# Optimization experiments

Hardware: AMD Instinct MI355X
Metric: run time of the kernel (lower is better)

## Reference

```python
import jax, jax.numpy as jnp
import numpy as np

B, S, H = 2, 2048, 4096
NQ, NKV, D = 32, 8, 128
EPS = 1e-6
THETA = 1000000.0


def rms_norm(x, w, eps=EPS):
    # normalize over last dim (per-head RMSNorm on head_dim)
    var = jnp.mean(jnp.square(x), axis=-1, keepdims=True)
    return x * jax.lax.rsqrt(var + eps) * w


def rope(x, positions, theta=THETA):
    # x: [B, S, N, D]; rotate-half convention (Qwen/Llama style)
    d = x.shape[-1]
    inv_freq = 1.0 / (theta ** (jnp.arange(0, d, 2, dtype=jnp.float32) / d))  # [D/2]
    ang = positions[:, None].astype(jnp.float32) * inv_freq[None, :]          # [S, D/2]
    cos = jnp.cos(ang)[None, :, None, :]
    sin = jnp.sin(ang)[None, :, None, :]
    x1, x2 = x[..., : d // 2], x[..., d // 2 :]
    return jnp.concatenate([x1 * cos - x2 * sin, x2 * cos + x1 * sin], axis=-1)


def setup_inputs() -> dict:
    key = jax.random.key(0)
    ks = jax.random.split(key, 7)
    sc_in = 1.0 / np.sqrt(H)
    sc_out = 1.0 / np.sqrt(NQ * D)
    return {
        "x": jax.random.normal(ks[0], (B, S, H), jnp.float32),
        "wq": jax.random.normal(ks[1], (H, NQ * D), jnp.float32) * sc_in,
        "wk": jax.random.normal(ks[2], (H, NKV * D), jnp.float32) * sc_in,
        "wv": jax.random.normal(ks[3], (H, NKV * D), jnp.float32) * sc_in,
        "wo": jax.random.normal(ks[4], (NQ * D, H), jnp.float32) * sc_out,
        "q_norm_w": jnp.ones((D,), jnp.float32),
        "k_norm_w": jnp.ones((D,), jnp.float32),
    }


def reference(x, wq, wk, wv, wo, q_norm_w, k_norm_w):
    b, s, _ = x.shape
    positions = jnp.arange(s)

    q = (x @ wq).reshape(b, s, NQ, D)   # [B,S,NQ,D]
    k = (x @ wk).reshape(b, s, NKV, D)  # [B,S,NKV,D]
    v = (x @ wv).reshape(b, s, NKV, D)

    # per-head QK RMSNorm, then RoPE
    q = rope(rms_norm(q, q_norm_w), positions)
    k = rope(rms_norm(k, k_norm_w), positions)

    # GQA: expand kv heads to query heads (group = NQ // NKV)
    g = NQ // NKV
    k = jnp.repeat(k, g, axis=2)  # [B,S,NQ,D]
    v = jnp.repeat(v, g, axis=2)

    scale = D ** -0.5
    scores = jnp.einsum("bqhd,bkhd->bhqk", q, k) * scale  # [B,NQ,S,S]
    causal = jnp.tril(jnp.ones((s, s), bool))
    scores = jnp.where(causal[None, None], scores, jnp.finfo(scores.dtype).min)
    attn = jax.nn.softmax(scores, axis=-1)

    out = jnp.einsum("bhqk,bkhd->bqhd", attn, v).reshape(b, s, NQ * D)
    return out @ wo
```

## Files before the change

kernel.cpp:

```cpp
#include <hip/hip_runtime.h>
#include <hip/hip_bf16.h>

#define DEV __device__ __forceinline__

typedef unsigned short u16;
typedef unsigned int u32;
typedef __attribute__((ext_vector_type(8))) short short8;
typedef __attribute__((ext_vector_type(4))) float f32x4;
typedef __attribute__((ext_vector_type(16))) float f32x16;

static constexpr int Bb = 2, Ss = 2048, Hh = 4096, NQ = 32, NKV = 8, Dd = 128;
static constexpr int Mm = Bb * Ss;

DEV u16 f2bf(float f) {
    u32 u = __float_as_uint(f);
    u32 r = (u + 0x7fffu + ((u >> 16) & 1u)) >> 16;
    return (u16)r;
}
DEV float bf2f(u16 b) { return __uint_as_float((u32)b << 16); }
DEV u32 cvtpk(float lo, float hi) {
    u32 r;
    asm("v_cvt_pk_bf16_f32 %0, %1, %2" : "=v"(r) : "v"(lo), "v"(hi));
    return r;
}

__global__ void k_cast(const float4* __restrict__ in, ushort4* __restrict__ out, int n4) {
    int i = blockIdx.x * 256 + threadIdx.x;
    if (i < n4) {
        float4 v = in[i];
        ushort4 o;
        o.x = f2bf(v.x); o.y = f2bf(v.y); o.z = f2bf(v.z); o.w = f2bf(v.w);
        out[i] = o;
    }
}

__global__ void k_transpose(const float* __restrict__ in, u16* __restrict__ out, int R, int C) {
    __shared__ float t[32][33];
    int lx = threadIdx.x & 31, ly = threadIdx.x >> 5;
    long tc = (long)blockIdx.x * 32, tr = (long)blockIdx.y * 32;
    #pragma unroll
    for (int i = 0; i < 32; i += 8) t[ly + i][lx] = in[(tr + ly + i) * C + tc + lx];
    __syncthreads();
    #pragma unroll
    for (int i = 0; i < 32; i += 8) out[(tc + ly + i) * R + tr + lx] = f2bf(t[lx][ly + i]);
}

DEV void gld16(const void* g, void* l) {
    __builtin_amdgcn_global_load_lds((const __attribute__((address_space(1))) void*)g,
                                     (__attribute__((address_space(3))) void*)l, 16, 0, 0);
}

#define FENCE asm volatile("" ::: "memory")

template <int MODE>
__global__ __launch_bounds__(512) void k_gemm256(const u16* __restrict__ A, const u16* __restrict__ B0,
                                                 const u16* __restrict__ B1, void* __restrict__ C0,
                                                 void* __restrict__ C1, void* __restrict__ C2,
                                                 int M, int N, int K, int nbx) {
    __shared__ u16 S[2][32768];
    const int tid = threadIdx.x, lane = tid & 63, wid = tid >> 6;
    const int wr = wid >> 2, wc = wid & 3;
    const int l = blockIdx.x;
    const int bx = l % nbx, by = l / nbx;
    const long m0 = (long)by * 256, n0 = (long)bx * 256;
    const int r15 = lane & 15;
    const int cch0 = 8 * ((lane >> 4) ^ (r15 & 7));

    const u16* Bbase = B0;
    long nb0 = n0;
    if (MODE == 3 && bx >= 16) { Bbase = B1; nb0 = n0 - 4096; }

    const u16 *pA[4], *pB[4];
    {
        int srow = wid * 8 + (lane >> 3);
        int scol = 8 * ((lane & 7) ^ (lane >> 3));
        #pragma unroll
        for (int j = 0; j < 4; j++) {
            pA[j] = A + (m0 + j * 64 + srow) * (long)K + scol;
            pB[j] = Bbase + (nb0 + j * 64 + srow) * (long)K + scol;
        }
    }

    f32x4 acc[8][4];
    #pragma unroll
    for (int i = 0; i < 8; i++)
        #pragma unroll
        for (int j = 0; j < 4; j++) acc[i][j] = f32x4{0.f, 0.f, 0.f, 0.f};

    const int NT = K / 64;
    auto STAGE_A = [&](int t) {
        int tb = t & 1; long ko = (long)t * 64;
        #pragma unroll
        for (int j = 0; j < 4; j++) gld16(pA[j] + ko, (void*)&S[tb][j * 4096 + wid * 512]);
    };
    auto STAGE_B = [&](int t) {
        int tb = t & 1; long ko = (long)t * 64;
        #pragma unroll
        for (int j = 0; j < 4; j++) gld16(pB[j] + ko, (void*)&S[tb][16384 + j * 4096 + wid * 512]);
    };

    const int aro = wr * 8192 + r15 * 64 + cch0;
    const int bro = 16384 + (wc >> 1) * 8192 + (wc & 1) * 4096 + r15 * 64 + cch0;

    STAGE_B(0); STAGE_A(0); STAGE_B(1); STAGE_A(1);
    asm volatile("s_waitcnt vmcnt(8)" ::: "memory");
    FENCE; __builtin_amdgcn_s_barrier(); FENCE;

    short8 af[4][2], b01[2][2], b23[2][2];
    for (int kt = 0; kt < NT; ++kt) {
        const u16* Sb = S[kt & 1];
        #pragma unroll
        for (int m = 0; m < 4; m++) {
            af[m][0] = *(const short8*)&Sb[aro + m * 1024];
            af[m][1] = *(const short8*)&Sb[(aro + m * 1024) ^ 32];
        }
        #pragma unroll
        for (int n = 0; n < 2; n++) {
            b01[n][0] = *(const short8*)&Sb[bro + n * 1024];
            b01[n][1] = *(const short8*)&Sb[(bro + n * 1024) ^ 32];
        }
        __builtin_amdgcn_s_setprio(1);
        #pragma unroll
        for (int m = 0; m < 4; m++)
            #pragma unroll
            for (int n = 0; n < 2; n++) {
                acc[m][n] = __builtin_amdgcn_mfma_f32_16x16x32_bf16(af[m][0], b01[n][0], acc[m][n], 0, 0, 0);
                acc[m][n] = __builtin_amdgcn_mfma_f32_16x16x32_bf16(af[m][1], b01[n][1], acc[m][n], 0, 0, 0);
            }
        __builtin_amdgcn_s_setprio(0);
        #pragma unroll
        for (int n = 0; n < 2; n++) {
            b23[n][0] = *(const short8*)&Sb[bro + (n + 2) * 1024];
            b23[n][1] = *(const short8*)&Sb[(bro + (n + 2) * 1024) ^ 32];
        }
        __builtin_amdgcn_s_setprio(1);
        #pragma unroll
        for (int m = 0; m < 4; m++)
            #pragma unroll
            for (int n = 0; n < 2; n++) {
                acc[m][n + 2] = __builtin_amdgcn_mfma_f32_16x16x32_bf16(af[m][0], b23[n][0], acc[m][n + 2], 0, 0, 0);
                acc[m][n + 2] = __builtin_amdgcn_mfma_f32_16x16x32_bf16(af[m][1], b23[n][1], acc[m][n + 2], 0, 0, 0);
            }
        __builtin_amdgcn_s_setprio(0);
        FENCE; __builtin_amdgcn_s_barrier(); FENCE;
        if (kt + 2 < NT) STAGE_B(kt + 2);
        #pragma unroll
        for (int m = 0; m < 4; m++) {
            af[m][0] = *(const short8*)&Sb[aro + (m + 4) * 1024];
            af[m][1] = *(const short8*)&Sb[(aro + (m + 4) * 1024) ^ 32];
        }
        __builtin_amdgcn_s_setprio(1);
        #pragma unroll
        for (int m = 0; m < 4; m++)
            #pragma unroll
            for (int n = 0; n < 2; n++) {
                acc[m + 4][n] = __builtin_amdgcn_mfma_f32_16x16x32_bf16(af[m][0], b01[n][0], acc[m + 4][n], 0, 0, 0);
                acc[m + 4][n] = __builtin_amdgcn_mfma_f32_16x16x32_bf16(af[m][1], b01[n][1], acc[m + 4][n], 0, 0, 0);
            }
        __builtin_amdgcn_s_setprio(0);
        FENCE; __builtin_amdgcn_s_barrier(); FENCE;
        if (kt + 2 < NT) {
            STAGE_A(kt + 2);
            asm volatile("s_waitcnt vmcnt(8)" ::: "memory");
        } else {
            asm volatile("s_waitcnt vmcnt(0)" ::: "memory");
        }
        __builtin_amdgcn_s_setprio(1);
        #pragma unroll
        for (int m = 0; m < 4; m++)
            #pragma unroll
            for (int n = 0; n < 2; n++) {
                acc[m + 4][n + 2] = __builtin_amdgcn_mfma_f32_16x16x32_bf16(af[m][0], b23[n][0], acc[m + 4][n + 2], 0, 0, 0);
                acc[m + 4][n + 2] = __builtin_amdgcn_mfma_f32_16x16x32_bf16(af[m][1], b23[n][1], acc[m + 4][n + 2], 0, 0, 0);
            }
        __builtin_amdgcn_s_setprio(0);
        FENCE; __builtin_amdgcn_s_barrier(); FENCE;
    }

    const int rq = (lane >> 4) * 4;
    #pragma unroll
    for (int m = 0; m < 8; m++) {
        #pragma unroll
        for (int n = 0; n < 4; n++) {
            long row0 = m0 + wr * 128 + m * 16 + rq;
            long col = n0 + wc * 64 + n * 16 + r15;
            if (MODE == 0) {
                float* Cf = (float*)C0;
                #pragma unroll
                for (int i = 0; i < 4; i++) Cf[(row0 + i) * N + col] = acc[m][n][i];
            } else if (MODE == 2) {
                u16* Cb = (u16*)C0;
                #pragma unroll
                for (int i = 0; i < 4; i++) Cb[(row0 + i) * N + col] = f2bf(acc[m][n][i]);
            } else {
                if (bx < 16) {
                    u16* Cb = (u16*)C0;
                    #pragma unroll
                    for (int i = 0; i < 4; i++) Cb[(row0 + i) * 4096 + col] = f2bf(acc[m][n][i]);
                } else if (bx < 20) {
                    u16* Cb = (u16*)C1;
                    long cl = col - 4096;
                    #pragma unroll
                    for (int i = 0; i < 4; i++) Cb[(row0 + i) * 1024 + cl] = f2bf(acc[m][n][i]);
                } else {
                    u16* Cb = (u16*)C2;
                    long cl = col - 5120;
                    ushort4 pk;
                    pk.x = f2bf(acc[m][n][0]);
                    pk.y = f2bf(acc[m][n][1]);
                    pk.z = f2bf(acc[m][n][2]);
                    pk.w = f2bf(acc[m][n][3]);
                    *(ushort4*)&Cb[cl * Mm + row0] = pk;
                }
            }
        }
    }
}

__global__ __launch_bounds__(256) void k_normrope(u16* __restrict__ buf,
                                                  const float* __restrict__ w, int NH, float oscale) {
    int row = blockIdx.x * 4 + (threadIdx.x >> 6);
    int lane = threadIdx.x & 63;
    long base = (long)row * 128;
    float x1 = bf2f(buf[base + lane]), x2 = bf2f(buf[base + lane + 64]);
    float ss = x1 * x1 + x2 * x2;
    #pragma unroll
    for (int m = 1; m < 64; m <<= 1) ss += __shfl_xor(ss, m);
    float r = rsqrtf(ss * (1.f / 128.f) + 1e-6f);
    float n1 = x1 * r * w[lane], n2 = x2 * r * w[lane + 64];
    int pos = (row / NH) % Ss;
    float invf = exp2f((float)lane * (-19.931568569324174f / 64.f));
    float ang = (float)pos * invf;
    float c = cosf(ang), sn = sinf(ang);
    buf[base + lane] = f2bf((n1 * c - n2 * sn) * oscale);
    buf[base + lane + 64] = f2bf((n2 * c + n1 * sn) * oscale);
}

__global__ __launch_bounds__(256, 2) void k_attn(const u16* __restrict__ Q, const u16* __restrict__ Kb,
                                                 const u16* __restrict__ Vg, u16* __restrict__ O) {
    __shared__ u16 KT[2][64 * 128];
    __shared__ u16 VT[2][128 * 64];
    int tid = threadIdx.x, lane = tid & 63, wid = tid >> 6;
    int d0 = blockIdx.x;
    int L = (d0 & 7) * 64 + (d0 >> 3);
    int pr = L & 31;
    int hk = (L >> 5) & 7;
    int b = L >> 8;
    int h = hk * 4 + wid;
    int q0a = pr * 32;
    int q0b = (63 - pr) * 32;
    int c31 = lane & 31, hi5 = lane >> 5;
    int kx16 = (c31 & 15) << 3;
    int kx8 = (c31 & 7) << 3;

    short8 qfa[8], qfb[8];
    {
        const u16* qra = Q + ((long)(b * Ss + q0a + c31) * NQ + h) * Dd + hi5 * 8;
        const u16* qrb = Q + ((long)(b * Ss + q0b + c31) * NQ + h) * Dd + hi5 * 8;
        #pragma unroll
        for (int c = 0; c < 8; c++) {
            qfa[c] = *(const short8*)(qra + c * 16);
            qfb[c] = *(const short8*)(qrb + c * 16);
        }
    }

    const u16* kg[4];
    const u16* vg[4];
    int i0 = wid * 4;
    #pragma unroll
    for (int ii = 0; ii < 4; ii++) {
        int i = i0 + ii;
        int r = i * 4 + (lane >> 4);
        kg[ii] = Kb + ((long)(b * Ss + r) * NKV + hk) * Dd + 8 * ((lane & 15) ^ (r & 15));
        int d = i * 8 + (lane >> 3);
        vg[ii] = Vg + (long)(hk * Dd + d) * Mm + (long)b * Ss + 8 * ((lane & 7) ^ (d & 7));
    }

    f32x16 oaa[4], oab[4];
    #pragma unroll
    for (int f = 0; f < 4; f++)
        #pragma unroll
        for (int r = 0; r < 16; r++) { oaa[f][r] = 0.f; oab[f][r] = 0.f; }
    float mra = -INFINITY, lra = 0.f, mrb = -INFINITY, lrb = 0.f;

    const long kadv = (long)64 * NKV * Dd;
    int nt = q0b / 64 + 1;
    int cur = 0;

    auto STEP = [&](int k0, int q0, const short8 (&qf)[8], f32x16 (&oa)[4],
                    float& mrun, float& lrun) {
        int ql = q0 + c31;
        int krow = k0 & 32;
        f32x16 st;
        #pragma unroll
        for (int r = 0; r < 16; r++) st[r] = 0.f;
        __builtin_amdgcn_s_setprio(1);
        #pragma unroll
        for (int c = 0; c < 8; c++) {
            short8 kf = *(const short8*)&KT[cur][(krow + c31) * 128 + ((c * 16 + hi5 * 8) ^ kx16)];
            st = __builtin_amdgcn_mfma_f32_32x32x16_bf16(kf, qf[c], st, 0, 0, 0);
        }
        __builtin_amdgcn_s_setprio(0);
        float p[16];
        if (k0 + 31 > q0) {
            #pragma unroll
            for (int r = 0; r < 16; r++) {
                int kidx = k0 + (r & 3) + 8 * (r >> 2) + 4 * hi5;
                p[r] = (kidx > ql) ? -INFINITY : st[r];
            }
        } else {
            #pragma unroll
            for (int r = 0; r < 16; r++) p[r] = st[r];
        }
        float pmax = p[0];
        #pragma unroll
        for (int r = 1; r < 16; r++) pmax = fmaxf(pmax, p[r]);
        pmax = fmaxf(pmax, __shfl_xor(pmax, 32));
        if (!__all(pmax - mrun <= 8.f)) {
            float mnew = fmaxf(mrun, pmax);
            float sc = __builtin_amdgcn_exp2f(mrun - mnew);
            lrun *= sc;
            #pragma unroll
            for (int f = 0; f < 4; f++)
                #pragma unroll
                for (int r = 0; r < 16; r++) oa[f][r] *= sc;
            mrun = mnew;
        }
        float ls = 0.f;
        #pragma unroll
        for (int r = 0; r < 16; r++) {
            float e = __builtin_amdgcn_exp2f(p[r] - mrun);
            p[r] = e;
            ls += e;
        }
        ls += __shfl_xor(ls, 32);
        lrun += ls;

        u32 w0 = cvtpk(p[0], p[1]), w1 = cvtpk(p[2], p[3]);
        u32 w2 = cvtpk(p[4], p[5]), w3 = cvtpk(p[6], p[7]);
        u32 w4 = cvtpk(p[8], p[9]), w5 = cvtpk(p[10], p[11]);
        u32 w6 = cvtpk(p[12], p[13]), w7 = cvtpk(p[14], p[15]);
        u32 x0 = (u32)__shfl_xor((int)w0, 32), x1 = (u32)__shfl_xor((int)w1, 32);
        u32 x2 = (u32)__shfl_xor((int)w2, 32), x3 = (u32)__shfl_xor((int)w3, 32);
        u32 x4 = (u32)__shfl_xor((int)w4, 32), x5 = (u32)__shfl_xor((int)w5, 32);
        u32 x6 = (u32)__shfl_xor((int)w6, 32), x7 = (u32)__shfl_xor((int)w7, 32);
        union { u32 u[4]; short8 s; } pb0, pb1;
        if (hi5) {
            pb0.u[0] = x2; pb0.u[1] = x3; pb0.u[2] = w2; pb0.u[3] = w3;
            pb1.u[0] = x6; pb1.u[1] = x7; pb1.u[2] = w6; pb1.u[3] = w7;
        } else {
            pb0.u[0] = w0; pb0.u[1] = w1; pb0.u[2] = x0; pb0.u[3] = x1;
            pb1.u[0] = w4; pb1.u[1] = w5; pb1.u[2] = x4; pb1.u[3] = x5;
        }
        __builtin_amdgcn_s_setprio(1);
        #pragma unroll
        for (int f = 0; f < 4; f++) {
            int d = 32 * f + c31;
            const u16* vrow = &VT[cur][d * 64];
            short8 v0 = *(const short8*)&vrow[(krow + hi5 * 8) ^ kx8];
            short8 v1 = *(const short8*)&vrow[(krow + 16 + hi5 * 8) ^ kx8];
            oa[f] = __builtin_amdgcn_mfma_f32_32x32x16_bf16(v0, pb0.s, oa[f], 0, 0, 0);
            oa[f] = __builtin_amdgcn_mfma_f32_32x32x16_bf16(v1, pb1.s, oa[f], 0, 0, 0);
        }
        __builtin_amdgcn_s_setprio(0);
    };

    #pragma unroll
    for (int ii = 0; ii < 4; ii++) {
        gld16(kg[ii], &KT[0][(i0 + ii) * 512]);
        gld16(vg[ii], &VT[0][(i0 + ii) * 512]);
    }
    __syncthreads();

    for (int t = 0; t < nt; ++t) {
        if (t + 1 < nt) {
            long ko = (long)(t + 1) * kadv;
            int vo = (t + 1) * 64;
            #pragma unroll
            for (int ii = 0; ii < 4; ii++) {
                gld16(kg[ii] + ko, &KT[cur ^ 1][(i0 + ii) * 512]);
                gld16(vg[ii] + vo, &VT[cur ^ 1][(i0 + ii) * 512]);
            }
        }
        #pragma unroll
        for (int ks = 0; ks < 2; ++ks) {
            int k0 = t * 64 + ks * 32;
            if (k0 <= q0a + 31) STEP(k0, q0a, qfa, oaa, mra, lra);
            if (k0 <= q0b + 31) STEP(k0, q0b, qfb, oab, mrb, lrb);
        }
        __syncthreads();
        cur ^= 1;
    }

    #pragma unroll
    for (int x = 0; x < 2; x++) {
        int q0 = x ? q0b : q0a;
        f32x16* oa = x ? oab : oaa;
        float linv = 1.f / (x ? lrb : lra);
        u16* orow = O + ((long)(b * Ss + q0 + c31) * NQ + h) * Dd;
        #pragma unroll
        for (int f = 0; f < 4; f++) {
            #pragma unroll
            for (int rq = 0; rq < 4; rq++) {
                int dbase = 32 * f + 8 * rq + 4 * hi5;
                union { u32 u[2]; ushort4 v; } pk;
                pk.u[0] = cvtpk(oa[f][4 * rq + 0] * linv, oa[f][4 * rq + 1] * linv);
                pk.u[1] = cvtpk(oa[f][4 * rq + 2] * linv, oa[f][4 * rq + 3] * linv);
                *(ushort4*)(orow + dbase) = pk.v;
            }
        }
    }
}

extern "C" void kernel_launch(void* const* d_in, const int* in_sizes, int n_in,
                              void* d_out, int out_size, void* d_ws, size_t ws_size,
                              hipStream_t stream) {
    (void)in_sizes; (void)n_in; (void)out_size; (void)ws_size;
    const float* x = (const float*)d_in[0];
    const float* wq = (const float*)d_in[1];
    const float* wk = (const float*)d_in[2];
    const float* wv = (const float*)d_in[3];
    const float* wo = (const float*)d_in[4];
    const float* qnw = (const float*)d_in[5];
    const float* knw = (const float*)d_in[6];

    char* ws = (char*)d_ws;
    const size_t MB = 1024 * 1024;
    const float qscale = (float)(0.08838834764831845 * 1.4426950408889634);

    u16* xb = (u16*)(ws);
    u16* Wq = (u16*)(ws + 32 * MB);
    u16* qb = (u16*)(ws + 64 * MB);
    u16* kb = (u16*)(ws + 96 * MB);
    u16* vt = (u16*)(ws + 104 * MB);
    u16* ao = xb;
    u16* Wkv = (u16*)(ws + 112 * MB);
    u16* WkT = Wkv;
    u16* WvT = Wkv + (size_t)1024 * 4096;

    int n4 = Mm * Hh / 4;
    k_cast<<<n4 / 256, 256, 0, stream>>>((const float4*)x, (ushort4*)xb, n4);

    k_transpose<<<dim3(Hh / 32, Hh / 32), 256, 0, stream>>>(wq, Wq, Hh, Hh);
    k_transpose<<<dim3((NKV * Dd) / 32, Hh / 32), 256, 0, stream>>>(wk, WkT, Hh, NKV * Dd);
    k_transpose<<<dim3((NKV * Dd) / 32, Hh / 32), 256, 0, stream>>>(wv, WvT, Hh, NKV * Dd);

    k_gemm256<3><<<24 * (Mm / 256), 512, 0, stream>>>(xb, Wq, Wkv, qb, kb, vt, Mm, 6144, Hh, 24);

    k_normrope<<<(Mm * NQ) / 4, 256, 0, stream>>>(qb, qnw, NQ, qscale);
    k_normrope<<<(Mm * NKV) / 4, 256, 0, stream>>>(kb, knw, NKV, 1.0f);

    k_attn<<<512, 256, 0, stream>>>(qb, kb, vt, ao);

    k_transpose<<<dim3(Hh / 32, Hh / 32), 256, 0, stream>>>(wo, Wq, Hh, Hh);
    k_gemm256<0><<<16 * (Mm / 256), 512, 0, stream>>>(ao, Wq, nullptr, d_out, nullptr, nullptr, Mm, Hh, NQ * Dd, 16);
}
```

Measured before the change: 552.1 us.

## Use 256x192 tiles for fused QKV GEMM with contiguous concatenated weight buffer

The QKV projection GEMM now uses a 256x192 output tile (NF=3 fragments per wave column) instead of 256x256, which raises the grid from 384 to 512 blocks. That gives a whole number of waves on the CU count and better load balance. Wq, Wk and Wv are transposed into one contiguous buffer, so the second B pointer and the bx-based branch are gone and output routing is done per column. The K loop is simplified from four MFMA phases to three, and the vmcnt wait count is parameterised. The trade-off is lower arithmetic intensity per block and more total A-tile reloads.

New measurement: 540.4 us. 1.02x faster.

```diff
diff --git a/kernel.cpp b/kernel.cpp
--- a/kernel.cpp
+++ b/kernel.cpp
@@ -54,59 +54,57 @@
 
 template <int MODE>
 __global__ __launch_bounds__(512) void k_gemm256(const u16* __restrict__ A, const u16* __restrict__ B0,
-                                                 const u16* __restrict__ B1, void* __restrict__ C0,
-                                                 void* __restrict__ C1, void* __restrict__ C2,
-                                                 int M, int N, int K, int nbx) {
-    __shared__ u16 S[2][32768];
+                                                 void* __restrict__ C0, void* __restrict__ C1,
+                                                 void* __restrict__ C2, int M, int N, int K, int nbx) {
+    constexpr int NF = (MODE == 3) ? 3 : 4;
+    constexpr int LPT = 4 + NF;
+    __shared__ u16 S[2][16384 + NF * 4096];
     const int tid = threadIdx.x, lane = tid & 63, wid = tid >> 6;
     const int wr = wid >> 2, wc = wid & 3;
     const int l = blockIdx.x;
     const int bx = l % nbx, by = l / nbx;
-    const long m0 = (long)by * 256, n0 = (long)bx * 256;
+    const long m0 = (long)by * 256, n0 = (long)bx * (NF * 64);
     const int r15 = lane & 15;
     const int cch0 = 8 * ((lane >> 4) ^ (r15 & 7));
 
-    const u16* Bbase = B0;
-    long nb0 = n0;
-    if (MODE == 3 && bx >= 16) { Bbase = B1; nb0 = n0 - 4096; }
-
-    const u16 *pA[4], *pB[4];
+    const u16 *pA[4], *pB[NF];
     {
-        int srow = wid * 8 + (lane >> 3);
-        int scol = 8 * ((lane & 7) ^ (lane >> 3));
-        #pragma unroll
-        for (int j = 0; j < 4; j++) {
-            pA[j] = A + (m0 + j * 64 + srow) * (long)K + scol;
-            pB[j] = Bbase + (nb0 + j * 64 + srow) * (long)K + scol;
-        }
-    }
-
-    f32x4 acc[8][4];
+        int rl = lane >> 3;
+        int sc = 8 * ((lane & 7) ^ rl);
+        #pragma unroll
+        for (int j = 0; j < 4; j++)
+            pA[j] = A + (m0 + (wid * 4 + j) * 8 + rl) * (long)K + sc;
+        #pragma unroll
+        for (int j = 0; j < NF; j++)
+            pB[j] = B0 + (n0 + (wid * NF + j) * 8 + rl) * (long)K + sc;
+    }
+
+    f32x4 acc[8][NF];
     #pragma unroll
     for (int i = 0; i < 8; i++)
         #pragma unroll
-        for (int j = 0; j < 4; j++) acc[i][j] = f32x4{0.f, 0.f, 0.f, 0.f};
+        for (int j = 0; j < NF; j++) acc[i][j] = f32x4{0.f, 0.f, 0.f, 0.f};
 
     const int NT = K / 64;
     auto STAGE_A = [&](int t) {
         int tb = t & 1; long ko = (long)t * 64;
         #pragma unroll
-        for (int j = 0; j < 4; j++) gld16(pA[j] + ko, (void*)&S[tb][j * 4096 + wid * 512]);
+        for (int j = 0; j < 4; j++) gld16(pA[j] + ko, (void*)&S[tb][(wid * 4 + j) * 512]);
     };
     auto STAGE_B = [&](int t) {
         int tb = t & 1; long ko = (long)t * 64;
         #pragma unroll
-        for (int j = 0; j < 4; j++) gld16(pB[j] + ko, (void*)&S[tb][16384 + j * 4096 + wid * 512]);
+        for (int j = 0; j < NF; j++) gld16(pB[j] + ko, (void*)&S[tb][16384 + (wid * NF + j) * 512]);
     };
 
     const int aro = wr * 8192 + r15 * 64 + cch0;
-    const int bro = 16384 + (wc >> 1) * 8192 + (wc & 1) * 4096 + r15 * 64 + cch0;
+    const int bro = 16384 + wc * (NF * 1024) + r15 * 64 + cch0;
 
     STAGE_B(0); STAGE_A(0); STAGE_B(1); STAGE_A(1);
-    asm volatile("s_waitcnt vmcnt(8)" ::: "memory");
+    asm volatile("s_waitcnt vmcnt(%0)" ::"i"(LPT) : "memory");
     FENCE; __builtin_amdgcn_s_barrier(); FENCE;
 
-    short8 af[4][2], b01[2][2], b23[2][2];
+    short8 af[4][2], bf[NF][2];
     for (int kt = 0; kt < NT; ++kt) {
         const u16* Sb = S[kt & 1];
         #pragma unroll
@@ -115,31 +113,17 @@
             af[m][1] = *(const short8*)&Sb[(aro + m * 1024) ^ 32];
         }
         #pragma unroll
-        for (int n = 0; n < 2; n++) {
-            b01[n][0] = *(const short8*)&Sb[bro + n * 1024];
-            b01[n][1] = *(const short8*)&Sb[(bro + n * 1024) ^ 32];
+        for (int n = 0; n < NF; n++) {
+            bf[n][0] = *(const short8*)&Sb[bro + n * 1024];
+            bf[n][1] = *(const short8*)&Sb[(bro + n * 1024) ^ 32];
         }
         __builtin_amdgcn_s_setprio(1);
         #pragma unroll
         for (int m = 0; m < 4; m++)
             #pragma unroll
-            for (int n = 0; n < 2; n++) {
-                acc[m][n] = __builtin_amdgcn_mfma_f32_16x16x32_bf16(af[m][0], b01[n][0], acc[m][n], 0, 0, 0);
-                acc[m][n] = __builtin_amdgcn_mfma_f32_16x16x32_bf16(af[m][1], b01[n][1], acc[m][n], 0, 0, 0);
-            }
-        __builtin_amdgcn_s_setprio(0);
-        #pragma unroll
-        for (int n = 0; n < 2; n++) {
-            b23[n][0] = *(const short8*)&Sb[bro + (n + 2) * 1024];
-            b23[n][1] = *(const short8*)&Sb[(bro + (n + 2) * 1024) ^ 32];
-        }
-        __builtin_amdgcn_s_setprio(1);
-        #pragma unroll
-        for (int m = 0; m < 4; m++)
-            #pragma unroll
-            for (int n = 0; n < 2; n++) {
-                acc[m][n + 2] = __builtin_amdgcn_mfma_f32_16x16x32_bf16(af[m][0], b23[n][0], acc[m][n + 2], 0, 0, 0);
-                acc[m][n + 2] = __builtin_amdgcn_mfma_f32_16x16x32_bf16(af[m][1], b23[n][1], acc[m][n + 2], 0, 0, 0);
+            for (int n = 0; n < NF; n++) {
+                acc[m][n] = __builtin_amdgcn_mfma_f32_16x16x32_bf16(af[m][0], bf[n][0], acc[m][n], 0, 0, 0);
+                acc[m][n] = __builtin_amdgcn_mfma_f32_16x16x32_bf16(af[m][1], bf[n][1], acc[m][n], 0, 0, 0);
             }
         __builtin_amdgcn_s_setprio(0);
         FENCE; __builtin_amdgcn_s_barrier(); FENCE;
@@ -153,27 +137,18 @@
         #pragma unroll
         for (int m = 0; m < 4; m++)
             #pragma unroll
-            for (int n = 0; n < 2; n++) {
-                acc[m + 4][n] = __builtin_amdgcn_mfma_f32_16x16x32_bf16(af[m][0], b01[n][0], acc[m + 4][n], 0, 0, 0);
-                acc[m + 4][n] = __builtin_amdgcn_mfma_f32_16x16x32_bf16(af[m][1], b01[n][1], acc[m + 4][n], 0, 0, 0);
+            for (int n = 0; n < NF; n++) {
+                acc[m + 4][n] = __builtin_amdgcn_mfma_f32_16x16x32_bf16(af[m][0], bf[n][0], acc[m + 4][n], 0, 0, 0);
+                acc[m + 4][n] = __builtin_amdgcn_mfma_f32_16x16x32_bf16(af[m][1], bf[n][1], acc[m + 4][n], 0, 0, 0);
             }
         __builtin_amdgcn_s_setprio(0);
         FENCE; __builtin_amdgcn_s_barrier(); FENCE;
         if (kt + 2 < NT) {
             STAGE_A(kt + 2);
-            asm volatile("s_waitcnt vmcnt(8)" ::: "memory");
+            asm volatile("s_waitcnt vmcnt(%0)" ::"i"(LPT) : "memory");
         } else {
             asm volatile("s_waitcnt vmcnt(0)" ::: "memory");
         }
-        __builtin_amdgcn_s_setprio(1);
-        #pragma unroll
-        for (int m = 0; m < 4; m++)
-            #pragma unroll
-            for (int n = 0; n < 2; n++) {
-                acc[m + 4][n + 2] = __builtin_amdgcn_mfma_f32_16x16x32_bf16(af[m][0], b23[n][0], acc[m + 4][n + 2], 0, 0, 0);
-                acc[m + 4][n + 2] = __builtin_amdgcn_mfma_f32_16x16x32_bf16(af[m][1], b23[n][1], acc[m + 4][n + 2], 0, 0, 0);
-            }
-        __builtin_amdgcn_s_setprio(0);
         FENCE; __builtin_amdgcn_s_barrier(); FENCE;
     }
 
@@ -181,23 +156,19 @@
     #pragma unroll
     for (int m = 0; m < 8; m++) {
         #pragma unroll
-        for (int n = 0; n < 4; n++) {
+        for (int n = 0; n < NF; n++) {
             long row0 = m0 + wr * 128 + m * 16 + rq;
-            long col = n0 + wc * 64 + n * 16 + r15;
+            long col = n0 + wc * (NF * 16) + n * 16 + r15;
             if (MODE == 0) {
                 float* Cf = (float*)C0;
                 #pragma unroll
                 for (int i = 0; i < 4; i++) Cf[(row0 + i) * N + col] = acc[m][n][i];
-            } else if (MODE == 2) {
-                u16* Cb = (u16*)C0;
-                #pragma unroll
-                for (int i = 0; i < 4; i++) Cb[(row0 + i) * N + col] = f2bf(acc[m][n][i]);
             } else {
-                if (bx < 16) {
+                if (col < 4096) {
                     u16* Cb = (u16*)C0;
                     #pragma unroll
                     for (int i = 0; i < 4; i++) Cb[(row0 + i) * 4096 + col] = f2bf(acc[m][n][i]);
-                } else if (bx < 20) {
+                } else if (col < 5120) {
                     u16* Cb = (u16*)C1;
                     long cl = col - 4096;
                     #pragma unroll
@@ -429,29 +400,27 @@
     const float qscale = (float)(0.08838834764831845 * 1.4426950408889634);
 
     u16* xb = (u16*)(ws);
-    u16* Wq = (u16*)(ws + 32 * MB);
-    u16* qb = (u16*)(ws + 64 * MB);
-    u16* kb = (u16*)(ws + 96 * MB);
-    u16* vt = (u16*)(ws + 104 * MB);
+    u16* Wqkv = (u16*)(ws + 32 * MB);
+    u16* qb = (u16*)(ws + 80 * MB);
+    u16* kb = (u16*)(ws + 112 * MB);
+    u16* vt = (u16*)(ws + 120 * MB);
     u16* ao = xb;
-    u16* Wkv = (u16*)(ws + 112 * MB);
-    u16* WkT = Wkv;
-    u16* WvT = Wkv + (size_t)1024 * 4096;
+    u16* WoT = Wqkv;
 
     int n4 = Mm * Hh / 4;
     k_cast<<<n4 / 256, 256, 0, stream>>>((const float4*)x, (ushort4*)xb, n4);
 
-    k_transpose<<<dim3(Hh / 32, Hh / 32), 256, 0, stream>>>(wq, Wq, Hh, Hh);
-    k_transpose<<<dim3((NKV * Dd) / 32, Hh / 32), 256, 0, stream>>>(wk, WkT, Hh, NKV * Dd);
-    k_transpose<<<dim3((NKV * Dd) / 32, Hh / 32), 256, 0, stream>>>(wv, WvT, Hh, NKV * Dd);
-
-    k_gemm256<3><<<24 * (Mm / 256), 512, 0, stream>>>(xb, Wq, Wkv, qb, kb, vt, Mm, 6144, Hh, 24);
+    k_transpose<<<dim3(Hh / 32, Hh / 32), 256, 0, stream>>>(wq, Wqkv, Hh, Hh);
+    k_transpose<<<dim3((NKV * Dd) / 32, Hh / 32), 256, 0, stream>>>(wk, Wqkv + (size_t)4096 * Hh, Hh, NKV * Dd);
+    k_transpose<<<dim3((NKV * Dd) / 32, Hh / 32), 256, 0, stream>>>(wv, Wqkv + (size_t)5120 * Hh, Hh, NKV * Dd);
+
+    k_gemm256<3><<<32 * (Mm / 256), 512, 0, stream>>>(xb, Wqkv, qb, kb, vt, Mm, 6144, Hh, 32);
 
     k_normrope<<<(Mm * NQ) / 4, 256, 0, stream>>>(qb, qnw, NQ, qscale);
     k_normrope<<<(Mm * NKV) / 4, 256, 0, stream>>>(kb, knw, NKV, 1.0f);
 
     k_attn<<<512, 256, 0, stream>>>(qb, kb, vt, ao);
 
-    k_transpose<<<dim3(Hh / 32, Hh / 32), 256, 0, stream>>>(wo, Wq, Hh, Hh);
-    k_gemm256<0><<<16 * (Mm / 256), 512, 0, stream>>>(ao, Wq, nullptr, d_out, nullptr, nullptr, Mm, Hh, NQ * Dd, 16);
-}
+    k_transpose<<<dim3(Hh / 32, Hh / 32), 256, 0, stream>>>(wo, WoT, Hh, Hh);
+    k_gemm256<0><<<16 * (Mm / 256), 512, 0, stream>>>(ao, WoT, d_out, nullptr, nullptr, Mm, Hh, NQ * Dd, 16);
+}
```
